# Kernel optimization log

Measured on AMD Instinct MI355X. Metric: run time of the kernel, lower is better.

Reference implementation:

```python
import jax, jax.numpy as jnp
import numpy as np

N_QUBITS = 8
TRASH = 1
DEPTH = 2
DIM = 2 ** N_QUBITS  # 256

# Qiskit little-endian: amplitude index k has qubit 0 as LSB. Reshaping a
# 256-vector to (2,)*8 puts qubit (N-1-a) on tensor axis a (axis 0 = MSB).
# Observable j is SparsePauliOp with 'Z' at string pos j => Z on qubit N-1-j
# => tensor axis j. So exp_j = sum probs * (1 - 2*bit_axis_j).


def _rx(t):
    c = jnp.cos(t / 2).astype(jnp.complex64)
    ms = (-1j * jnp.sin(t / 2)).astype(jnp.complex64)
    return jnp.stack([jnp.stack([c, ms]), jnp.stack([ms, c])])


def _ry(t):
    c = jnp.cos(t / 2).astype(jnp.complex64)
    s = jnp.sin(t / 2).astype(jnp.complex64)
    return jnp.stack([jnp.stack([c, -s]), jnp.stack([s, c])])


def _rz(t):
    e = jnp.exp((-0.5j) * t.astype(jnp.complex64))
    z = jnp.zeros_like(e)
    return jnp.stack([jnp.stack([e, z]), jnp.stack([z, jnp.conj(e)])])


def _apply_1q(psi, U, q):
    ax = 1 + (N_QUBITS - 1 - q)
    return jnp.moveaxis(jnp.tensordot(psi, U, axes=([ax], [1])), -1, ax)


def _apply_cx(psi, c, t):
    axc = 1 + (N_QUBITS - 1 - c)
    axt = 1 + (N_QUBITS - 1 - t)
    shape = [1] * psi.ndim
    shape[axc] = 2
    ctrl = (jnp.arange(2).reshape(shape) == 1)
    return jnp.where(ctrl, jnp.flip(psi, axis=axt), psi)


def _r3_ansatz(psi, theta, nq, depth):
    k = 0
    for _ in range(depth):
        for q in range(nq):
            psi = _apply_1q(psi, _rx(theta[k + 0]), q)
            psi = _apply_1q(psi, _ry(theta[k + 1]), q)
            psi = _apply_1q(psi, _rz(theta[k + 2]), q)
            k += 3
        for q in range(nq - 1):  # linear entanglement
            psi = _apply_cx(psi, q, q + 1)
    return psi


# sign matrix for Z expectations: S[j, k] = 1 - 2*bit_{N-1-j}(k)
_k = np.arange(DIM)
_SIGNS = np.stack([1.0 - 2.0 * ((_k >> (N_QUBITS - 1 - j)) & 1)
                   for j in range(N_QUBITS)]).astype(np.float32)  # (8, 256)


def setup_inputs() -> dict:
    key = jax.random.key(0)
    k1, k2, k3, k4 = jax.random.split(key, 4)
    return {
        "x": jax.random.normal(k1, (32, 1024, 256), dtype=jnp.float32),
        "theta1": jax.random.normal(k2, (DEPTH * N_QUBITS * 3,), dtype=jnp.float32),
        "theta2": jax.random.normal(k3, (DEPTH * (N_QUBITS - TRASH) * 3,), dtype=jnp.float32),
        "theta3": jax.random.normal(k4, (DEPTH * N_QUBITS * 3,), dtype=jnp.float32),
    }


def reference(x, theta1, theta2, theta3):
    B, T, D = x.shape
    xf = x.reshape(B * T, D)
    # amplitude encode: normalize classical vector into quantum amplitudes
    norm = jnp.linalg.norm(xf, axis=1, keepdims=True)
    norm = jnp.where(norm == 0, jnp.float32(1e-8), norm)
    psi = (xf / norm).astype(jnp.complex64).reshape((B * T,) + (2,) * N_QUBITS)
    # ansatz: U1 (8q) -> U2 (7q) -> U3 (8q)
    psi = _r3_ansatz(psi, theta1, N_QUBITS, DEPTH)
    psi = _r3_ansatz(psi, theta2, N_QUBITS - TRASH, DEPTH)
    psi = _r3_ansatz(psi, theta3, N_QUBITS, DEPTH)
    # Z expectation on each observable
    probs = (jnp.abs(psi) ** 2).reshape(B * T, DIM)
    y = probs @ jnp.asarray(_SIGNS).T  # (B*T, 8)
    # amplitude decode: normalize, |.|^2, zero-pad to DIM
    yn = jnp.linalg.norm(y, axis=1, keepdims=True)
    yn = jnp.where(yn == 0, jnp.float32(1e-8), yn)
    cv = (y / yn) ** 2
    out = jnp.pad(cv, ((0, 0), (0, DIM - N_QUBITS)))
    return out.reshape(B, T, DIM)
```

## Files before the change

kernel.cpp:

```cpp
#include <hip/hip_runtime.h>
#include <math.h>


#define DEV __device__ __forceinline__

typedef __attribute__((ext_vector_type(8))) short short8;
typedef __attribute__((ext_vector_type(4))) float f32x4;

DEV float2 cmul(float2 a, float2 b) {
  return make_float2(a.x * b.x - a.y * b.y, a.x * b.y + a.y * b.x);
}
DEV float2 cadd(float2 a, float2 b) { return make_float2(a.x + b.x, a.y + b.y); }

DEV unsigned short bf_rne(float v) {
  unsigned u = __float_as_uint(v);
  return (unsigned short)((u + 0x7FFFu + ((u >> 16) & 1u)) >> 16);
}


struct Psi4 { float re[4]; float im[4]; };

template <int Q>
DEV void pair_gate(Psi4& s, const float2* __restrict__ Mlo,
                   const float2* __restrict__ Mhi, int lane) {
  const int b0 = (lane >> Q) & 1, b1 = (lane >> (Q + 1)) & 1;
  float2 lo_d = Mlo[b0 * 2 + b0];
  float2 lo_o = Mlo[b0 * 2 + (b0 ^ 1)];
  float2 hi_d = Mhi[b1 * 2 + b1];
  float2 hi_o = Mhi[b1 * 2 + (b1 ^ 1)];
  float2 c00 = cmul(hi_d, lo_d);
  float2 c01 = cmul(hi_d, lo_o);
  float2 c10 = cmul(hi_o, lo_d);
  float2 c11 = cmul(hi_o, lo_o);
  const int m0 = 1 << Q, m1 = 2 << Q;
#pragma unroll
  for (int r = 0; r < 4; ++r) {
    float ar = s.re[r], ai = s.im[r];
    float p0r = __shfl_xor(ar, m0, 64), p0i = __shfl_xor(ai, m0, 64);
    float p1r = __shfl_xor(ar, m1, 64), p1i = __shfl_xor(ai, m1, 64);
    float p2r = __shfl_xor(ar, m0 | m1, 64), p2i = __shfl_xor(ai, m0 | m1, 64);
    float nr = c00.x * ar - c00.y * ai + c01.x * p0r - c01.y * p0i
             + c10.x * p1r - c10.y * p1i + c11.x * p2r - c11.y * p2i;
    float ni = c00.x * ai + c00.y * ar + c01.x * p0i + c01.y * p0r
             + c10.x * p1i + c10.y * p1r + c11.x * p2i + c11.y * p2r;
    s.re[r] = nr; s.im[r] = ni;
  }
}

DEV void regpair_gate(Psi4& s, const float2* __restrict__ Mlo,
                      const float2* __restrict__ Mhi) {
  float nr[4], ni[4];
#pragma unroll
  for (int r = 0; r < 4; ++r) {
    const int b0 = r & 1, b1 = (r >> 1) & 1;
    float2 c00 = cmul(Mhi[b1 * 2 + b1], Mlo[b0 * 2 + b0]);
    float2 c01 = cmul(Mhi[b1 * 2 + b1], Mlo[b0 * 2 + (b0 ^ 1)]);
    float2 c10 = cmul(Mhi[b1 * 2 + (b1 ^ 1)], Mlo[b0 * 2 + b0]);
    float2 c11 = cmul(Mhi[b1 * 2 + (b1 ^ 1)], Mlo[b0 * 2 + (b0 ^ 1)]);
    nr[r] = c00.x * s.re[r] - c00.y * s.im[r]
          + c01.x * s.re[r ^ 1] - c01.y * s.im[r ^ 1]
          + c10.x * s.re[r ^ 2] - c10.y * s.im[r ^ 2]
          + c11.x * s.re[r ^ 3] - c11.y * s.im[r ^ 3];
    ni[r] = c00.x * s.im[r] + c00.y * s.re[r]
          + c01.x * s.im[r ^ 1] + c01.y * s.re[r ^ 1]
          + c10.x * s.im[r ^ 2] + c10.y * s.re[r ^ 2]
          + c11.x * s.im[r ^ 3] + c11.y * s.re[r ^ 3];
  }
#pragma unroll
  for (int r = 0; r < 4; ++r) { s.re[r] = nr[r]; s.im[r] = ni[r]; }
}

DEV void reg0_gate(Psi4& s, const float2* __restrict__ M) {
  float nr[4], ni[4];
#pragma unroll
  for (int r = 0; r < 4; ++r) {
    const int b = r & 1;
    float2 d = M[b * 2 + b], o = M[b * 2 + (b ^ 1)];
    nr[r] = d.x * s.re[r] - d.y * s.im[r] + o.x * s.re[r ^ 1] - o.y * s.im[r ^ 1];
    ni[r] = d.x * s.im[r] + d.y * s.re[r] + o.x * s.im[r ^ 1] + o.y * s.re[r ^ 1];
  }
#pragma unroll
  for (int r = 0; r < 4; ++r) { s.re[r] = nr[r]; s.im[r] = ni[r]; }
}

template <bool FULL8>
DEV void perm_cx(Psi4& s, int lane) {
  const int slane = (lane ^ (lane << 1)) & 63;
  const bool L5 = ((lane >> 5) & 1) != 0;
  float nr[4], ni[4];
#pragma unroll
  for (int r = 0; r < 4; ++r) {
    const int r0 = r & 1, r1 = (r >> 1) & 1;
    const int hiBit = FULL8 ? (r1 ^ r0) : r1;
    const int sA = (hiBit << 1) | r0;
    const int sB = sA ^ 1;
    float aRe = __shfl(s.re[sA], slane, 64);
    float aIm = __shfl(s.im[sA], slane, 64);
    float bRe = __shfl(s.re[sB], slane, 64);
    float bIm = __shfl(s.im[sB], slane, 64);
    nr[r] = L5 ? bRe : aRe;
    ni[r] = L5 ? bIm : aIm;
  }
#pragma unroll
  for (int r = 0; r < 4; ++r) { s.re[r] = nr[r]; s.im[r] = ni[r]; }
}

template <int NQ>
DEV void ansatz_f(Psi4& s, const float2* __restrict__ Mg, int lane) {
#pragma unroll
  for (int d = 0; d < 2; ++d) {
    const float2* Md = Mg + d * NQ * 4;
    pair_gate<0>(s, Md + 0, Md + 4, lane);
    pair_gate<2>(s, Md + 8, Md + 12, lane);
    pair_gate<4>(s, Md + 16, Md + 20, lane);
    if (NQ == 8) regpair_gate(s, Md + 24, Md + 28);
    else reg0_gate(s, Md + 24);
    perm_cx<NQ == 8>(s, lane);
  }
}

DEV void store_v(unsigned short* __restrict__ Vsw, int n, int kk, float v) {
  int k = kk >> 5, rem = kk & 31, quad = rem >> 3, jj = rem & 7;
  int nn = n & 255;
  int w = (nn >> 6) & 3, t = (nn >> 4) & 3, cl = nn & 15;
  int g = w * 8 + ((n >= 256) ? 4 + t : t);
  int L = quad * 16 + cl;
  unsigned short hi = bf_rne(v);
  float hif = __uint_as_float(((unsigned)hi) << 16);
  unsigned short lo = bf_rne(v - hif);
  size_t base = (size_t)k * 32768 + (size_t)g * 1024 + (size_t)L * 8 + jj;
  Vsw[base] = hi;
  Vsw[base + 512] = lo;
}

__global__ void build_u(const float* __restrict__ th1, const float* __restrict__ th2,
                        const float* __restrict__ th3, unsigned short* __restrict__ Vsw) {
  __shared__ float2 Mg[46 * 4];
  const int tid = threadIdx.x;
  if (tid < 46) {
    float thx, thy, thz;
    if (tid < 16)      { thx = th1[tid * 3]; thy = th1[tid * 3 + 1]; thz = th1[tid * 3 + 2]; }
    else if (tid < 30) { int u = (tid - 16) * 3; thx = th2[u]; thy = th2[u + 1]; thz = th2[u + 2]; }
    else               { int u = (tid - 30) * 3; thx = th3[u]; thy = th3[u + 1]; thz = th3[u + 2]; }
    float sx, cx_, sy, cy_, sz, cz_;
    sincosf(0.5f * thx, &sx, &cx_);
    sincosf(0.5f * thy, &sy, &cy_);
    sincosf(0.5f * thz, &sz, &cz_);
    float2 rx[4] = {{cx_, 0}, {0, -sx}, {0, -sx}, {cx_, 0}};
    float2 ry[4] = {{cy_, 0}, {-sy, 0}, {sy, 0}, {cy_, 0}};
    float2 A0 = cadd(cmul(ry[0], rx[0]), cmul(ry[1], rx[2]));
    float2 A1 = cadd(cmul(ry[0], rx[1]), cmul(ry[1], rx[3]));
    float2 A2 = cadd(cmul(ry[2], rx[0]), cmul(ry[3], rx[2]));
    float2 A3 = cadd(cmul(ry[2], rx[1]), cmul(ry[3], rx[3]));
    float2 ezm = make_float2(cz_, -sz), ezp = make_float2(cz_, sz);
    Mg[tid * 4 + 0] = cmul(ezm, A0);
    Mg[tid * 4 + 1] = cmul(ezm, A1);
    Mg[tid * 4 + 2] = cmul(ezp, A2);
    Mg[tid * 4 + 3] = cmul(ezp, A3);
  }
  __syncthreads();

  const int lane = tid & 63;
  const int j = blockIdx.x * 4 + (tid >> 6);
  Psi4 s;
#pragma unroll
  for (int r = 0; r < 4; ++r) {
    int a = (r << 6) | lane;
    s.re[r] = (a == j) ? 1.f : 0.f;
    s.im[r] = 0.f;
  }
  ansatz_f<8>(s, Mg, lane);
  ansatz_f<7>(s, Mg + 16 * 4, lane);
  ansatz_f<8>(s, Mg + 30 * 4, lane);
#pragma unroll
  for (int r = 0; r < 4; ++r) {
    int a = (r << 6) | lane;
    store_v(Vsw, a, j, s.re[r]);
    store_v(Vsw, a + 256, j, s.im[r]);
  }
}


DEV void split8(float4 f0, float4 f1, short8& h, short8& l) {
  float v0 = f0.x, v1 = f0.y, v2 = f0.z, v3 = f0.w;
  float v4 = f1.x, v5 = f1.y, v6 = f1.z, v7 = f1.w;
#define SPLIT1(i, v)                                            \
  {                                                             \
    unsigned u = __float_as_uint(v);                            \
    h[i] = (short)(u >> 16);                      \
    float hf = __uint_as_float(u & 0xFFFF0000u);                \
    l[i] = (short)(__float_as_uint((v) - hf) >> 16);            \
  }
  SPLIT1(0, v0) SPLIT1(1, v1) SPLIT1(2, v2) SPLIT1(3, v3)
  SPLIT1(4, v4) SPLIT1(5, v5) SPLIT1(6, v6) SPLIT1(7, v7)
#undef SPLIT1
}

__global__ __launch_bounds__(512, 4) void pqc_main(const float* __restrict__ x,
                                                   const unsigned short* __restrict__ Vsw,
                                                   float* __restrict__ out) {
  const int tid = threadIdx.x;
  const int ww = tid >> 6;
  const int w = ww & 3;
  const int h = ww >> 2;
  const int L = tid & 63;
  const int quad = L >> 4;
  const int c = L & 15;
  const int row0 = blockIdx.x * 64;

  __shared__ float part[4][64][8];
  __shared__ float ys[64][8];
  __shared__ float invn[64];

  f32x4 acc[2][8];
#pragma unroll
  for (int mt = 0; mt < 2; ++mt)
#pragma unroll
    for (int t = 0; t < 8; ++t) acc[mt][t] = (f32x4){0.f, 0.f, 0.f, 0.f};

  const float* xr0 = x + (size_t)(row0 + h * 32 + c) * 256 + quad * 8;
  const float* xr1 = xr0 + 16 * 256;
  const unsigned short* pb = Vsw + (size_t)w * 8192 + (size_t)L * 8;

#pragma unroll
  for (int k = 0; k < 8; ++k) {
    float4 a00 = *(const float4*)(xr0 + k * 32);
    float4 a01 = *(const float4*)(xr0 + k * 32 + 4);
    float4 a10 = *(const float4*)(xr1 + k * 32);
    float4 a11 = *(const float4*)(xr1 + k * 32 + 4);
    short8 ah0, al0, ah1, al1;
    split8(a00, a01, ah0, al0);
    split8(a10, a11, ah1, al1);
    const unsigned short* pk = pb + (size_t)k * 32768;
#pragma unroll
    for (int t = 0; t < 8; ++t) {
      short8 bh = *(const short8*)(pk + t * 1024);
      short8 bl = *(const short8*)(pk + t * 1024 + 512);
      acc[0][t] = __builtin_amdgcn_mfma_f32_16x16x32_bf16(ah0, bh, acc[0][t], 0, 0, 0);
      acc[0][t] = __builtin_amdgcn_mfma_f32_16x16x32_bf16(ah0, bl, acc[0][t], 0, 0, 0);
      acc[0][t] = __builtin_amdgcn_mfma_f32_16x16x32_bf16(al0, bh, acc[0][t], 0, 0, 0);
      acc[1][t] = __builtin_amdgcn_mfma_f32_16x16x32_bf16(ah1, bh, acc[1][t], 0, 0, 0);
      acc[1][t] = __builtin_amdgcn_mfma_f32_16x16x32_bf16(ah1, bl, acc[1][t], 0, 0, 0);
      acc[1][t] = __builtin_amdgcn_mfma_f32_16x16x32_bf16(al1, bh, acc[1][t], 0, 0, 0);
    }
  }

#pragma unroll
  for (int mt = 0; mt < 2; ++mt) {
#pragma unroll
    for (int r = 0; r < 4; ++r) {
      float p0 = acc[mt][0][r] * acc[mt][0][r] + acc[mt][4][r] * acc[mt][4][r];
      float p1 = acc[mt][1][r] * acc[mt][1][r] + acc[mt][5][r] * acc[mt][5][r];
      float p2 = acc[mt][2][r] * acc[mt][2][r] + acc[mt][6][r] * acc[mt][6][r];
      float p3 = acc[mt][3][r] * acc[mt][3][r] + acc[mt][7][r] * acc[mt][7][r];
      float s01 = p0 + p1, s23 = p2 + p3;
      float av = s01 + s23;
      float bv = s01 - s23;
      float cv = (p0 - p1) + (p2 - p3);
#pragma unroll
      for (int st = 0; st < 4; ++st) {
        int msk = 1 << st;
        float ta = __shfl_xor(av, msk, 64);
        av = ((c >> st) & 1) ? (ta - av) : (av + ta);
        bv += __shfl_xor(bv, msk, 64);
        cv += __shfl_xor(cv, msk, 64);
      }
      int m = h * 32 + mt * 16 + quad * 4 + r;
      if (c == 0) {
        part[w][m][0] = ((w >> 1) & 1) ? -av : av;
        part[w][m][1] = (w & 1) ? -av : av;
        part[w][m][2] = bv;
        part[w][m][3] = cv;
      } else if (c == 8) part[w][m][4] = av;
      else if (c == 4) part[w][m][5] = av;
      else if (c == 2) part[w][m][6] = av;
      else if (c == 1) part[w][m][7] = av;
    }
  }
  __syncthreads();

  {
    int m = tid >> 3, jj = tid & 7;
    ys[m][jj] = part[0][m][jj] + part[1][m][jj] + part[2][m][jj] + part[3][m][jj];
  }
  __syncthreads();

  if (tid < 64) {
    float n = 0.f;
#pragma unroll
    for (int jj = 0; jj < 8; ++jj) { float v = ys[tid][jj]; n = fmaf(v, v, n); }
    n = sqrtf(n);
    invn[tid] = (n == 0.f) ? 0.f : 1.f / n;
  }
  __syncthreads();

  float4* o4 = (float4*)(out + (size_t)row0 * 256);
#pragma unroll
  for (int i = 0; i < 8; ++i) {
    int e = i * 512 + tid;
    int row = e >> 6;
    int c4 = (e & 63) * 4;
    float4 v = make_float4(0.f, 0.f, 0.f, 0.f);
    if (c4 < 8) {
      float iv = invn[row];
      float t0 = ys[row][c4 + 0] * iv;
      float t1 = ys[row][c4 + 1] * iv;
      float t2 = ys[row][c4 + 2] * iv;
      float t3 = ys[row][c4 + 3] * iv;
      v = make_float4(t0 * t0, t1 * t1, t2 * t2, t3 * t3);
    }
    o4[e] = v;
  }
}

extern "C" void kernel_launch(void* const* d_in, const int* in_sizes, int n_in,
                              void* d_out, int out_size, void* d_ws, size_t ws_size,
                              hipStream_t stream) {
  const float* x = (const float*)d_in[0];
  const float* th1 = (const float*)d_in[1];
  const float* th2 = (const float*)d_in[2];
  const float* th3 = (const float*)d_in[3];
  float* out = (float*)d_out;
  unsigned short* Vsw = (unsigned short*)d_ws;

  build_u<<<64, 256, 0, stream>>>(th1, th2, th3, Vsw);
  pqc_main<<<512, 512, 0, stream>>>(x, Vsw, out);
}
```

Measured before the change: 129.9 us.

## Halve block to 4 waves with 64-row tiles and prefetch A/B operands

Each block now uses 4 waves instead of 8. Each wave computes all 64 rows (four 16-row M-tiles), so every loaded B (unitary) fragment feeds twice as many MFMAs and global traffic on Vsw drops. The x and B fragments for the next step are software-prefetched into registers to overlap loads with MFMA work. In exchange, accumulator register use doubles (128 floats) and there are fewer waves per block, which may cut occupancy and the latency hiding that comes with it.

```diff
diff --git a/kernel.cpp b/kernel.cpp
--- a/kernel.cpp
+++ b/kernel.cpp
@@ -182,8 +182,6 @@
 
 
 DEV void split8(float4 f0, float4 f1, short8& h, short8& l) {
-  float v0 = f0.x, v1 = f0.y, v2 = f0.z, v3 = f0.w;
-  float v4 = f1.x, v5 = f1.y, v6 = f1.z, v7 = f1.w;
 #define SPLIT1(i, v)                                            \
   {                                                             \
     unsigned u = __float_as_uint(v);                            \
@@ -191,18 +189,16 @@
     float hf = __uint_as_float(u & 0xFFFF0000u);                \
     l[i] = (short)(__float_as_uint((v) - hf) >> 16);            \
   }
-  SPLIT1(0, v0) SPLIT1(1, v1) SPLIT1(2, v2) SPLIT1(3, v3)
-  SPLIT1(4, v4) SPLIT1(5, v5) SPLIT1(6, v6) SPLIT1(7, v7)
+  SPLIT1(0, f0.x) SPLIT1(1, f0.y) SPLIT1(2, f0.z) SPLIT1(3, f0.w)
+  SPLIT1(4, f1.x) SPLIT1(5, f1.y) SPLIT1(6, f1.z) SPLIT1(7, f1.w)
 #undef SPLIT1
 }
 
-__global__ __launch_bounds__(512, 4) void pqc_main(const float* __restrict__ x,
+__global__ __launch_bounds__(256, 2) void pqc_main(const float* __restrict__ x,
                                                    const unsigned short* __restrict__ Vsw,
                                                    float* __restrict__ out) {
   const int tid = threadIdx.x;
-  const int ww = tid >> 6;
-  const int w = ww & 3;
-  const int h = ww >> 2;
+  const int w = tid >> 6;
   const int L = tid & 63;
   const int quad = L >> 4;
   const int c = L & 15;
@@ -212,41 +208,59 @@
   __shared__ float ys[64][8];
   __shared__ float invn[64];
 
-  f32x4 acc[2][8];
-#pragma unroll
-  for (int mt = 0; mt < 2; ++mt)
+  f32x4 acc[4][8];
+#pragma unroll
+  for (int mt = 0; mt < 4; ++mt)
 #pragma unroll
     for (int t = 0; t < 8; ++t) acc[mt][t] = (f32x4){0.f, 0.f, 0.f, 0.f};
 
-  const float* xr0 = x + (size_t)(row0 + h * 32 + c) * 256 + quad * 8;
-  const float* xr1 = xr0 + 16 * 256;
+  const float* xbase = x + (size_t)(row0 + c) * 256 + quad * 8;
   const unsigned short* pb = Vsw + (size_t)w * 8192 + (size_t)L * 8;
 
+  float4 araw[4][2];
+#pragma unroll
+  for (int mt = 0; mt < 4; ++mt) {
+    araw[mt][0] = *(const float4*)(xbase + mt * 4096);
+    araw[mt][1] = *(const float4*)(xbase + mt * 4096 + 4);
+  }
+  short8 bh = *(const short8*)(pb);
+  short8 bl = *(const short8*)(pb + 512);
+
 #pragma unroll
   for (int k = 0; k < 8; ++k) {
-    float4 a00 = *(const float4*)(xr0 + k * 32);
-    float4 a01 = *(const float4*)(xr0 + k * 32 + 4);
-    float4 a10 = *(const float4*)(xr1 + k * 32);
-    float4 a11 = *(const float4*)(xr1 + k * 32 + 4);
-    short8 ah0, al0, ah1, al1;
-    split8(a00, a01, ah0, al0);
-    split8(a10, a11, ah1, al1);
+    short8 ah[4], al[4];
+#pragma unroll
+    for (int mt = 0; mt < 4; ++mt) split8(araw[mt][0], araw[mt][1], ah[mt], al[mt]);
+    if (k < 7) {
+#pragma unroll
+      for (int mt = 0; mt < 4; ++mt) {
+        araw[mt][0] = *(const float4*)(xbase + mt * 4096 + (k + 1) * 32);
+        araw[mt][1] = *(const float4*)(xbase + mt * 4096 + (k + 1) * 32 + 4);
+      }
+    }
     const unsigned short* pk = pb + (size_t)k * 32768;
 #pragma unroll
     for (int t = 0; t < 8; ++t) {
-      short8 bh = *(const short8*)(pk + t * 1024);
-      short8 bl = *(const short8*)(pk + t * 1024 + 512);
-      acc[0][t] = __builtin_amdgcn_mfma_f32_16x16x32_bf16(ah0, bh, acc[0][t], 0, 0, 0);
-      acc[0][t] = __builtin_amdgcn_mfma_f32_16x16x32_bf16(ah0, bl, acc[0][t], 0, 0, 0);
-      acc[0][t] = __builtin_amdgcn_mfma_f32_16x16x32_bf16(al0, bh, acc[0][t], 0, 0, 0);
-      acc[1][t] = __builtin_amdgcn_mfma_f32_16x16x32_bf16(ah1, bh, acc[1][t], 0, 0, 0);
-      acc[1][t] = __builtin_amdgcn_mfma_f32_16x16x32_bf16(ah1, bl, acc[1][t], 0, 0, 0);
-      acc[1][t] = __builtin_amdgcn_mfma_f32_16x16x32_bf16(al1, bh, acc[1][t], 0, 0, 0);
+      short8 nbh, nbl;
+      if (t < 7) {
+        nbh = *(const short8*)(pk + (t + 1) * 1024);
+        nbl = *(const short8*)(pk + (t + 1) * 1024 + 512);
+      } else if (k < 7) {
+        nbh = *(const short8*)(pk + 32768);
+        nbl = *(const short8*)(pk + 32768 + 512);
+      }
+#pragma unroll
+      for (int mt = 0; mt < 4; ++mt) {
+        acc[mt][t] = __builtin_amdgcn_mfma_f32_16x16x32_bf16(ah[mt], bh, acc[mt][t], 0, 0, 0);
+        acc[mt][t] = __builtin_amdgcn_mfma_f32_16x16x32_bf16(ah[mt], bl, acc[mt][t], 0, 0, 0);
+        acc[mt][t] = __builtin_amdgcn_mfma_f32_16x16x32_bf16(al[mt], bh, acc[mt][t], 0, 0, 0);
+      }
+      if (t < 7 || k < 7) { bh = nbh; bl = nbl; }
     }
   }
 
 #pragma unroll
-  for (int mt = 0; mt < 2; ++mt) {
+  for (int mt = 0; mt < 4; ++mt) {
 #pragma unroll
     for (int r = 0; r < 4; ++r) {
       float p0 = acc[mt][0][r] * acc[mt][0][r] + acc[mt][4][r] * acc[mt][4][r];
@@ -265,7 +279,7 @@
         bv += __shfl_xor(bv, msk, 64);
         cv += __shfl_xor(cv, msk, 64);
       }
-      int m = h * 32 + mt * 16 + quad * 4 + r;
+      int m = mt * 16 + quad * 4 + r;
       if (c == 0) {
         part[w][m][0] = ((w >> 1) & 1) ? -av : av;
         part[w][m][1] = (w & 1) ? -av : av;
@@ -279,8 +293,10 @@
   }
   __syncthreads();
 
-  {
-    int m = tid >> 3, jj = tid & 7;
+#pragma unroll
+  for (int s = 0; s < 2; ++s) {
+    int e = s * 256 + tid;
+    int m = e >> 3, jj = e & 7;
     ys[m][jj] = part[0][m][jj] + part[1][m][jj] + part[2][m][jj] + part[3][m][jj];
   }
   __syncthreads();
@@ -296,8 +312,8 @@
 
   float4* o4 = (float4*)(out + (size_t)row0 * 256);
 #pragma unroll
-  for (int i = 0; i < 8; ++i) {
-    int e = i * 512 + tid;
+  for (int i = 0; i < 16; ++i) {
+    int e = i * 256 + tid;
     int row = e >> 6;
     int c4 = (e & 63) * 4;
     float4 v = make_float4(0.f, 0.f, 0.f, 0.f);
@@ -324,5 +340,5 @@
   unsigned short* Vsw = (unsigned short*)d_ws;
 
   build_u<<<64, 256, 0, stream>>>(th1, th2, th3, Vsw);
-  pqc_main<<<512, 512, 0, stream>>>(x, Vsw, out);
-}
+  pqc_main<<<512, 256, 0, stream>>>(x, Vsw, out);
+}
```

Result: no change. 128.8 us (-0.8%).

## Stage split bf16 activations in LDS and retile waves over all 64 rows

Applied to the files above, without the earlier changes.

Input rows are loaded once per block, split into high and low bf16 halves and stored in shared memory in MFMA operand layout. Each of the 8 waves now covers all 64 rows (4 M-tiles) but only half of its former N range (real or imaginary half), instead of 32 rows with both halves. This reuses each B fragment loaded from global memory across 4 M-tiles rather than 2, halving the B traffic per wave, and removes the redundant per-wave splitting of the same activations. The cost is an extra LDS staging pass with a barrier, LDS reads of A fragments, more accumulator registers live at once, and an 8-way partial reduction in the epilogue.

```diff
diff --git a/kernel.cpp b/kernel.cpp
--- a/kernel.cpp
+++ b/kernel.cpp
@@ -181,78 +181,92 @@
 }
 
 
-DEV void split8(float4 f0, float4 f1, short8& h, short8& l) {
-  float v0 = f0.x, v1 = f0.y, v2 = f0.z, v3 = f0.w;
-  float v4 = f1.x, v5 = f1.y, v6 = f1.z, v7 = f1.w;
-#define SPLIT1(i, v)                                            \
-  {                                                             \
-    unsigned u = __float_as_uint(v);                            \
-    h[i] = (short)(u >> 16);                      \
-    float hf = __uint_as_float(u & 0xFFFF0000u);                \
-    l[i] = (short)(__float_as_uint((v) - hf) >> 16);            \
-  }
-  SPLIT1(0, v0) SPLIT1(1, v1) SPLIT1(2, v2) SPLIT1(3, v3)
-  SPLIT1(4, v4) SPLIT1(5, v5) SPLIT1(6, v6) SPLIT1(7, v7)
-#undef SPLIT1
-}
-
 __global__ __launch_bounds__(512, 4) void pqc_main(const float* __restrict__ x,
                                                    const unsigned short* __restrict__ Vsw,
                                                    float* __restrict__ out) {
   const int tid = threadIdx.x;
   const int ww = tid >> 6;
-  const int w = ww & 3;
-  const int h = ww >> 2;
+  const int w = ww >> 1;
+  const int half = ww & 1;
   const int L = tid & 63;
   const int quad = L >> 4;
   const int c = L & 15;
   const int row0 = blockIdx.x * 64;
 
-  __shared__ float part[4][64][8];
+  __shared__ unsigned short A2[2][8][4][512];
   __shared__ float ys[64][8];
   __shared__ float invn[64];
-
-  f32x4 acc[2][8];
-#pragma unroll
-  for (int mt = 0; mt < 2; ++mt)
-#pragma unroll
-    for (int t = 0; t < 8; ++t) acc[mt][t] = (f32x4){0.f, 0.f, 0.f, 0.f};
-
-  const float* xr0 = x + (size_t)(row0 + h * 32 + c) * 256 + quad * 8;
-  const float* xr1 = xr0 + 16 * 256;
-  const unsigned short* pb = Vsw + (size_t)w * 8192 + (size_t)L * 8;
+  float* part = (float*)&A2[0][0][0][0];
+
+  {
+    const float4* xsrc = (const float4*)(x + (size_t)row0 * 256);
+#pragma unroll
+    for (int i = 0; i < 8; ++i) {
+      int e = i * 512 + tid;
+      int row = e >> 6;
+      int kk = (e & 63) * 4;
+      float4 f = xsrc[e];
+      ushort4 h, l;
+#define SPLIT1(fld, v)                                           \
+      {                                                          \
+        unsigned u = __float_as_uint(v);                         \
+        h.fld = (unsigned short)(u >> 16);         \
+        float hf = __uint_as_float(u & 0xFFFF0000u);             \
+        l.fld = (unsigned short)(__float_as_uint((v) - hf) >> 16); \
+      }
+      SPLIT1(x, f.x) SPLIT1(y, f.y) SPLIT1(z, f.z) SPLIT1(w, f.w)
+#undef SPLIT1
+      int mt = row >> 4, cc = row & 15;
+      int k = kk >> 5, q = (kk >> 3) & 3, j = kk & 7;
+      int idx = (q * 16 + cc) * 8 + j;
+      *(ushort4*)&A2[0][k][mt][idx] = h;
+      *(ushort4*)&A2[1][k][mt][idx] = l;
+    }
+  }
+  __syncthreads();
+
+  f32x4 acc[4][4];
+#pragma unroll
+  for (int mt = 0; mt < 4; ++mt)
+#pragma unroll
+    for (int tt = 0; tt < 4; ++tt) acc[mt][tt] = (f32x4){0.f, 0.f, 0.f, 0.f};
+
+  const unsigned short* pb = Vsw + (size_t)w * 8192 + (size_t)half * 4096 + (size_t)L * 8;
 
 #pragma unroll
   for (int k = 0; k < 8; ++k) {
-    float4 a00 = *(const float4*)(xr0 + k * 32);
-    float4 a01 = *(const float4*)(xr0 + k * 32 + 4);
-    float4 a10 = *(const float4*)(xr1 + k * 32);
-    float4 a11 = *(const float4*)(xr1 + k * 32 + 4);
-    short8 ah0, al0, ah1, al1;
-    split8(a00, a01, ah0, al0);
-    split8(a10, a11, ah1, al1);
+    short8 ah[4], al[4];
+#pragma unroll
+    for (int mt = 0; mt < 4; ++mt) {
+      ah[mt] = *(const short8*)&A2[0][k][mt][L * 8];
+      al[mt] = *(const short8*)&A2[1][k][mt][L * 8];
+    }
     const unsigned short* pk = pb + (size_t)k * 32768;
 #pragma unroll
-    for (int t = 0; t < 8; ++t) {
-      short8 bh = *(const short8*)(pk + t * 1024);
-      short8 bl = *(const short8*)(pk + t * 1024 + 512);
-      acc[0][t] = __builtin_amdgcn_mfma_f32_16x16x32_bf16(ah0, bh, acc[0][t], 0, 0, 0);
-      acc[0][t] = __builtin_amdgcn_mfma_f32_16x16x32_bf16(ah0, bl, acc[0][t], 0, 0, 0);
-      acc[0][t] = __builtin_amdgcn_mfma_f32_16x16x32_bf16(al0, bh, acc[0][t], 0, 0, 0);
-      acc[1][t] = __builtin_amdgcn_mfma_f32_16x16x32_bf16(ah1, bh, acc[1][t], 0, 0, 0);
-      acc[1][t] = __builtin_amdgcn_mfma_f32_16x16x32_bf16(ah1, bl, acc[1][t], 0, 0, 0);
-      acc[1][t] = __builtin_amdgcn_mfma_f32_16x16x32_bf16(al1, bh, acc[1][t], 0, 0, 0);
-    }
-  }
-
-#pragma unroll
-  for (int mt = 0; mt < 2; ++mt) {
+    for (int tt = 0; tt < 4; ++tt) {
+      short8 bh = *(const short8*)(pk + tt * 1024);
+      short8 bl = *(const short8*)(pk + tt * 1024 + 512);
+#pragma unroll
+      for (int mt = 0; mt < 4; ++mt)
+        acc[mt][tt] = __builtin_amdgcn_mfma_f32_16x16x32_bf16(ah[mt], bh, acc[mt][tt], 0, 0, 0);
+#pragma unroll
+      for (int mt = 0; mt < 4; ++mt)
+        acc[mt][tt] = __builtin_amdgcn_mfma_f32_16x16x32_bf16(ah[mt], bl, acc[mt][tt], 0, 0, 0);
+#pragma unroll
+      for (int mt = 0; mt < 4; ++mt)
+        acc[mt][tt] = __builtin_amdgcn_mfma_f32_16x16x32_bf16(al[mt], bh, acc[mt][tt], 0, 0, 0);
+    }
+  }
+  __syncthreads();
+
+#pragma unroll
+  for (int mt = 0; mt < 4; ++mt) {
 #pragma unroll
     for (int r = 0; r < 4; ++r) {
-      float p0 = acc[mt][0][r] * acc[mt][0][r] + acc[mt][4][r] * acc[mt][4][r];
-      float p1 = acc[mt][1][r] * acc[mt][1][r] + acc[mt][5][r] * acc[mt][5][r];
-      float p2 = acc[mt][2][r] * acc[mt][2][r] + acc[mt][6][r] * acc[mt][6][r];
-      float p3 = acc[mt][3][r] * acc[mt][3][r] + acc[mt][7][r] * acc[mt][7][r];
+      float p0 = acc[mt][0][r] * acc[mt][0][r];
+      float p1 = acc[mt][1][r] * acc[mt][1][r];
+      float p2 = acc[mt][2][r] * acc[mt][2][r];
+      float p3 = acc[mt][3][r] * acc[mt][3][r];
       float s01 = p0 + p1, s23 = p2 + p3;
       float av = s01 + s23;
       float bv = s01 - s23;
@@ -265,23 +279,27 @@
         bv += __shfl_xor(bv, msk, 64);
         cv += __shfl_xor(cv, msk, 64);
       }
-      int m = h * 32 + mt * 16 + quad * 4 + r;
+      int m = mt * 16 + quad * 4 + r;
+      float* pm = part + (ww * 64 + m) * 8;
       if (c == 0) {
-        part[w][m][0] = ((w >> 1) & 1) ? -av : av;
-        part[w][m][1] = (w & 1) ? -av : av;
-        part[w][m][2] = bv;
-        part[w][m][3] = cv;
-      } else if (c == 8) part[w][m][4] = av;
-      else if (c == 4) part[w][m][5] = av;
-      else if (c == 2) part[w][m][6] = av;
-      else if (c == 1) part[w][m][7] = av;
+        pm[0] = ((w >> 1) & 1) ? -av : av;
+        pm[1] = (w & 1) ? -av : av;
+        pm[2] = bv;
+        pm[3] = cv;
+      } else if (c == 8) pm[4] = av;
+      else if (c == 4) pm[5] = av;
+      else if (c == 2) pm[6] = av;
+      else if (c == 1) pm[7] = av;
     }
   }
   __syncthreads();
 
   {
     int m = tid >> 3, jj = tid & 7;
-    ys[m][jj] = part[0][m][jj] + part[1][m][jj] + part[2][m][jj] + part[3][m][jj];
+    float s = 0.f;
+#pragma unroll
+    for (int p = 0; p < 8; ++p) s += part[(p * 64 + m) * 8 + jj];
+    ys[m][jj] = s;
   }
   __syncthreads();
 
```

After: 126.9 us. 2.3% less time.
